# Performance work log

Measured on AMD Instinct MI355X. Metric: run time of the kernel, lower is better.

The kernel has to match this reference:

```python
import jax, jax.numpy as jnp
import numpy as np

INPUT_DIM = 1024
HIDDEN_DIM = 1024
BATCH = 8
SEQ = 2048


def setup_inputs() -> dict:
    key = jax.random.key(0)
    ks = jax.random.split(key, 7)
    s = 1.0 / np.sqrt(INPUT_DIM)
    return {
        "subgraph_embeddings": jax.random.normal(ks[0], (BATCH, SEQ, INPUT_DIM), dtype=jnp.float32),
        "Wq": jax.random.uniform(ks[1], (INPUT_DIM, HIDDEN_DIM), jnp.float32, -s, s),
        "bq": jax.random.uniform(ks[2], (HIDDEN_DIM,), jnp.float32, -s, s),
        "Wk": jax.random.uniform(ks[3], (INPUT_DIM, HIDDEN_DIM), jnp.float32, -s, s),
        "bk": jax.random.uniform(ks[4], (HIDDEN_DIM,), jnp.float32, -s, s),
        "Wv": jax.random.uniform(ks[5], (INPUT_DIM, HIDDEN_DIM), jnp.float32, -s, s),
        "bv": jax.random.uniform(ks[6], (HIDDEN_DIM,), jnp.float32, -s, s),
    }


def reference(subgraph_embeddings, Wq, bq, Wk, bk, Wv, bv):
    x = subgraph_embeddings  # [B, S, D]
    Q = jnp.einsum('bsd,dh->bsh', x, Wq) + bq
    K = jnp.einsum('bsd,dh->bsh', x, Wk) + bk
    V = jnp.einsum('bsd,dh->bsh', x, Wv) + bv
    scale = jnp.sqrt(jnp.float32(HIDDEN_DIM))
    scores = jnp.einsum('bqh,bkh->bqk', Q, K) / scale  # [B, S, S]
    weights = jax.nn.softmax(scores, axis=-1)
    return jnp.einsum('bqk,bkh->bqh', weights, V)
```

## Files before the change

### kernel.cpp

```cpp
#include <hip/hip_runtime.h>
#include <hip/hip_bf16.h>
#include <stdint.h>

typedef unsigned short u16;
typedef unsigned int u32;
typedef __attribute__((ext_vector_type(8))) short bf16x8;
typedef __attribute__((ext_vector_type(4))) float f32x4;

#define S_LEN 2048
#define D_DIM 1024
#define H_DIM 1024
#define BATCH 8
#define M_TOTAL (BATCH * S_LEN)

__device__ __forceinline__ u16 f2b(float f) {
  u32 u = __builtin_bit_cast(u32, f);
  u32 r = (u + 0x7fffu + ((u >> 16) & 1u)) >> 16;
  return (u16)r;
}

__global__ __launch_bounds__(256) void cast_x_kernel(const float* __restrict__ in,
                                                     u16* __restrict__ out, int n8) {
  int i = blockIdx.x * 256 + threadIdx.x;
  if (i >= n8) return;
  const float4* p = (const float4*)in;
  float4 a = p[2 * i], b = p[2 * i + 1];
  u32 w0 = (u32)f2b(a.x) | ((u32)f2b(a.y) << 16);
  u32 w1 = (u32)f2b(a.z) | ((u32)f2b(a.w) << 16);
  u32 w2 = (u32)f2b(b.x) | ((u32)f2b(b.y) << 16);
  u32 w3 = (u32)f2b(b.z) | ((u32)f2b(b.w) << 16);
  ((uint4*)out)[i] = make_uint4(w0, w1, w2, w3);
}

__global__ __launch_bounds__(256) void wcast_all_kernel(
    const float* __restrict__ Wq, const float* __restrict__ Wk,
    const float* __restrict__ Wv, const float* __restrict__ bq,
    const float* __restrict__ bk, u16* __restrict__ Wtqk,
    u16* __restrict__ Wtv, float* __restrict__ bqk, float* __restrict__ lsum) {
  __shared__ float tile[32][33];
  int z = blockIdx.z;
  const float* W = (z == 0) ? Wq : (z == 1) ? Wk : Wv;
  u16* Wt = (z == 0) ? Wtqk : (z == 1) ? (Wtqk + 1024 * 1024) : Wtv;
  int h0 = blockIdx.x * 32, d0 = blockIdx.y * 32;
  int tx = threadIdx.x & 31, ty = threadIdx.x >> 5;
#pragma unroll
  for (int r = ty; r < 32; r += 8)
    tile[r][tx] = W[(size_t)(d0 + r) * H_DIM + h0 + tx];
  if (blockIdx.x == 0 && blockIdx.y == 0) {
    if (z == 0) {
      for (int i = threadIdx.x; i < 1024; i += 256) bqk[i] = bq[i];
    } else if (z == 1) {
      for (int i = threadIdx.x; i < 1024; i += 256) bqk[1024 + i] = bk[i];
    } else {
      for (int i = threadIdx.x; i < M_TOTAL; i += 256) lsum[i] = 0.f;
    }
  }
  __syncthreads();
#pragma unroll
  for (int r = ty; r < 32; r += 8)
    Wt[(size_t)(h0 + r) * D_DIM + d0 + tx] = f2b(tile[tx][r]);
}

template <int BIAS, int EPI, bool OUT_BF16>
__global__ __launch_bounds__(512, 2) void gemm256(
    const u16* __restrict__ A, const u16* __restrict__ Bt, void* __restrict__ Cout,
    const float* __restrict__ bias, float* __restrict__ lsum,
    int M, int N, int K, int lda, int ldb, int ldc,
    long long aBatch, long long bBatch, long long cBatch, float scale) {
  __shared__ __align__(16) u16 As[2][256 * 64];
  __shared__ __align__(16) u16 Bs[2][256 * 64];
  const int tid = threadIdx.x;
  const int wave = tid >> 6, lane = tid & 63;
  const int quad = lane >> 4, lr = lane & 15;
  const int wm = (wave >> 2) * 128, wn = (wave & 3) * 64;
  const int row0 = blockIdx.x * 256, col0 = blockIdx.y * 256;
  A += (size_t)blockIdx.z * (size_t)aBatch;
  Bt += (size_t)blockIdx.z * (size_t)bBatch;

  f32x4 acc[8][4] = {};

  auto AsL = (__attribute__((address_space(3))) char*)&As[0][0];
  auto BsL = (__attribute__((address_space(3))) char*)&Bs[0][0];
  const char* Ab = (const char*)A;
  const char* Bb = (const char*)Bt;

  auto stage_aq = [&](int buf, int q, int k0) {
#pragma unroll
    for (int rr = 0; rr < 2; ++rr) {
      int idx = rr * 512 + tid;
      int i = idx >> 3, ch = idx & 7;
      int row = ((i >> 6) << 7) | (q << 6) | (i & 63);
      int cs = ch ^ (row & 7);
      const void* g = Ab + (((size_t)(row0 + row) * lda + (size_t)(k0 + cs * 8)) * 2);
      __builtin_amdgcn_global_load_lds(
          (const __attribute__((address_space(1))) void*)g,
          (__attribute__((address_space(3))) void*)(AsL + (size_t)buf * 32768 +
                                                   (size_t)(row * 8 + ch) * 16),
          16, 0, 0);
    }
  };
  auto stage_bq = [&](int buf, int q, int k0) {
#pragma unroll
    for (int rr = 0; rr < 2; ++rr) {
      int idx = rr * 512 + tid;
      int i = idx >> 3, ch = idx & 7;
      int row = ((i >> 5) << 6) | (q << 5) | (i & 31);
      int cs = ch ^ (row & 7);
      const void* g = Bb + (((size_t)(col0 + row) * ldb + (size_t)(k0 + cs * 8)) * 2);
      __builtin_amdgcn_global_load_lds(
          (const __attribute__((address_space(1))) void*)g,
          (__attribute__((address_space(3))) void*)(BsL + (size_t)buf * 32768 +
                                                   (size_t)(row * 8 + ch) * 16),
          16, 0, 0);
    }
  };

#define READ_A(MH)                                                              \
  _Pragma("unroll") for (int ksi = 0; ksi < 2; ++ksi)                           \
  _Pragma("unroll") for (int i = 0; i < 4; ++i) {                               \
    int r = wm + ((MH) * 4 + i) * 16 + lr;                                      \
    int cc = (ksi * 4 + quad) ^ (r & 7);                                        \
    afr[ksi][i] = *(const bf16x8*)&As[cur][r * 64 + cc * 8];                    \
  }
#define READ_B(NH)                                                              \
  _Pragma("unroll") for (int ksi = 0; ksi < 2; ++ksi)                           \
  _Pragma("unroll") for (int j = 0; j < 2; ++j) {                               \
    int r = wn + ((NH) * 2 + j) * 16 + lr;                                      \
    int cc = (ksi * 4 + quad) ^ (r & 7);                                        \
    bfr[NH][j][ksi] = *(const bf16x8*)&Bs[cur][r * 64 + cc * 8];                \
  }
#define MFMA_QUAD(MH, NH)                                                       \
  _Pragma("unroll") for (int ksi = 0; ksi < 2; ++ksi)                           \
  _Pragma("unroll") for (int i = 0; i < 4; ++i)                                 \
  _Pragma("unroll") for (int j = 0; j < 2; ++j)                                 \
    acc[(MH) * 4 + i][(NH) * 2 + j] = __builtin_amdgcn_mfma_f32_16x16x32_bf16(  \
        afr[ksi][i], bfr[NH][j][ksi], acc[(MH) * 4 + i][(NH) * 2 + j], 0, 0, 0);

#define BAR() __builtin_amdgcn_s_barrier()
#define WAIT_LGKM0()                                       \
  asm volatile("s_waitcnt lgkmcnt(0)" ::: "memory");       \
  __builtin_amdgcn_sched_barrier(0)
#define PRIO1() __builtin_amdgcn_s_setprio(1)
#define PRIO0() __builtin_amdgcn_s_setprio(0)

  const int nkt = K >> 6;

  stage_aq(0, 0, 0); stage_bq(0, 0, 0); stage_bq(0, 1, 0); stage_aq(0, 1, 0);
  stage_aq(1, 0, 64); stage_bq(1, 0, 64); stage_bq(1, 1, 64);
  asm volatile("s_waitcnt vmcnt(6)" ::: "memory");
  __builtin_amdgcn_sched_barrier(0);
  BAR();

  bf16x8 afr[2][4];
  bf16x8 bfr[2][2][2];

  for (int t = 0; t <= nkt - 3; ++t) {
    const int cur = t & 1, nxt = cur ^ 1;
    const int kn1 = (t + 1) << 6, kn2 = (t + 2) << 6;
    READ_A(0);
    READ_B(0);
    stage_aq(nxt, 1, kn1);
    asm volatile("s_waitcnt lgkmcnt(8)" ::: "memory");
    BAR();
    WAIT_LGKM0();
    PRIO1(); MFMA_QUAD(0, 0); PRIO0();
    BAR();
    READ_B(1);
    stage_aq(cur, 0, kn2);
    BAR();
    WAIT_LGKM0();
    PRIO1(); MFMA_QUAD(0, 1); PRIO0();
    BAR();
    READ_A(1);
    stage_bq(cur, 0, kn2);
    BAR();
    WAIT_LGKM0();
    PRIO1(); MFMA_QUAD(1, 0); PRIO0();
    BAR();
    stage_bq(cur, 1, kn2);
    BAR();
    PRIO1(); MFMA_QUAD(1, 1); PRIO0();
    asm volatile("s_waitcnt vmcnt(6)" ::: "memory");
    __builtin_amdgcn_sched_barrier(0);
    BAR();
  }
  {
    const int t = nkt - 2;
    const int cur = t & 1, nxt = cur ^ 1;
    const int kn1 = (t + 1) << 6;
    READ_A(0);
    READ_B(0);
    stage_aq(nxt, 1, kn1);
    asm volatile("s_waitcnt lgkmcnt(8)" ::: "memory");
    BAR();
    WAIT_LGKM0();
    PRIO1(); MFMA_QUAD(0, 0); PRIO0();
    BAR();
    READ_B(1);
    BAR();
    WAIT_LGKM0();
    PRIO1(); MFMA_QUAD(0, 1); PRIO0();
    BAR();
    READ_A(1);
    BAR();
    WAIT_LGKM0();
    PRIO1(); MFMA_QUAD(1, 0); PRIO0();
    BAR();
    PRIO1(); MFMA_QUAD(1, 1); PRIO0();
    asm volatile("s_waitcnt vmcnt(0)" ::: "memory");
    __builtin_amdgcn_sched_barrier(0);
    BAR();
  }
  {
    const int cur = (nkt - 1) & 1;
    READ_A(0);
    READ_B(0);
    MFMA_QUAD(0, 0);
    READ_B(1);
    MFMA_QUAD(0, 1);
    READ_A(1);
    MFMA_QUAD(1, 0);
    MFMA_QUAD(1, 1);
  }
#undef READ_A
#undef READ_B
#undef MFMA_QUAD
#undef BAR
#undef WAIT_LGKM0
#undef PRIO1
#undef PRIO0

  const long long lrow0 = (long long)blockIdx.z * M + row0;

  if constexpr (EPI == 1) {
    u16* C = (u16*)Cout + (size_t)blockIdx.z * (size_t)cBatch;
#pragma unroll
    for (int i = 0; i < 8; ++i) {
#pragma unroll
      for (int ii = 0; ii < 4; ++ii) {
        int r = wm + i * 16 + quad * 4 + ii;
        float rowsum = 0.f;
#pragma unroll
        for (int j = 0; j < 4; ++j) {
          float e = __expf(acc[i][j][ii] * scale);
          rowsum += e;
          C[(size_t)(row0 + r) * ldc + (col0 + wn + j * 16 + lr)] = f2b(e);
        }
#pragma unroll
        for (int off = 1; off < 16; off <<= 1) rowsum += __shfl_xor(rowsum, off);
        if (lr == 0) atomicAdd(lsum + lrow0 + r, rowsum);
      }
    }
    return;
  }

#pragma unroll
  for (int i = 0; i < 8; ++i) {
#pragma unroll
    for (int ii = 0; ii < 4; ++ii) {
      int r = wm + i * 16 + quad * 4 + ii;
      float radd = 0.f, rmul = 1.f;
      if (BIAS == 2) radd = bias[row0 + r];
      if (EPI == 2) rmul = 1.0f / lsum[lrow0 + r];
#pragma unroll
      for (int j = 0; j < 4; ++j) {
        int c = col0 + wn + j * 16 + lr;
        float v = acc[i][j][ii] * rmul + radd;
        if (BIAS == 1) v += bias[c];
        if constexpr (OUT_BF16) {
          u16* C = (u16*)Cout + (size_t)blockIdx.z * (size_t)cBatch;
          C[(size_t)(row0 + r) * ldc + c] = f2b(v);
        } else {
          float* C = (float*)Cout + (size_t)blockIdx.z * (size_t)cBatch;
          C[(size_t)(row0 + r) * ldc + c] = v;
        }
      }
    }
  }
}

extern "C" void kernel_launch(void* const* d_in, const int* in_sizes, int n_in,
                              void* d_out, int out_size, void* d_ws, size_t ws_size,
                              hipStream_t stream) {
  const float* x = (const float*)d_in[0];
  const float* Wq = (const float*)d_in[1];
  const float* bq = (const float*)d_in[2];
  const float* Wk = (const float*)d_in[3];
  const float* bk = (const float*)d_in[4];
  const float* Wv = (const float*)d_in[5];
  const float* bv = (const float*)d_in[6];
  float* out = (float*)d_out;

  char* ws = (char*)d_ws;
  u16* xb = (u16*)ws;   ws += (size_t)M_TOTAL * D_DIM * 2;
  u16* Wtqk = (u16*)ws; ws += (size_t)2 * H_DIM * D_DIM * 2;
  u16* Wtv = (u16*)ws;  ws += (size_t)H_DIM * D_DIM * 2;
  u16* QKm = (u16*)ws;  ws += (size_t)M_TOTAL * 2 * H_DIM * 2;
  u16* Vt = (u16*)ws;   ws += (size_t)BATCH * H_DIM * S_LEN * 2;
  u16* Sm = (u16*)ws;   ws += (size_t)BATCH * S_LEN * S_LEN * 2;
  float* bqk = (float*)ws;  ws += 2048 * 4;
  float* lsum = (float*)ws; ws += (size_t)M_TOTAL * 4;

  cast_x_kernel<<<(M_TOTAL * D_DIM / 8 + 255) / 256, 256, 0, stream>>>(
      x, xb, M_TOTAL * D_DIM / 8);
  wcast_all_kernel<<<dim3(32, 32, 3), 256, 0, stream>>>(
      Wq, Wk, Wv, bq, bk, Wtqk, Wtv, bqk, lsum);

  gemm256<1, 0, true><<<dim3(64, 8, 1), 512, 0, stream>>>(
      xb, Wtqk, QKm, bqk, nullptr, M_TOTAL, 2 * H_DIM, D_DIM,
      D_DIM, D_DIM, 2 * H_DIM, 0, 0, 0, 0.f);

  gemm256<2, 0, true><<<dim3(4, 8, BATCH), 512, 0, stream>>>(
      Wtv, xb, Vt, bv, nullptr, H_DIM, S_LEN, D_DIM,
      D_DIM, D_DIM, S_LEN,
      0LL, (long long)S_LEN * D_DIM, (long long)H_DIM * S_LEN, 0.f);

  gemm256<0, 1, true><<<dim3(8, 8, BATCH), 512, 0, stream>>>(
      QKm, QKm + H_DIM, Sm, nullptr, lsum, S_LEN, S_LEN, H_DIM,
      2 * H_DIM, 2 * H_DIM, S_LEN,
      (long long)S_LEN * 2 * H_DIM, (long long)S_LEN * 2 * H_DIM,
      (long long)S_LEN * S_LEN, 0.03125f);

  gemm256<0, 2, false><<<dim3(8, 4, BATCH), 512, 0, stream>>>(
      Sm, Vt, out, nullptr, lsum, S_LEN, H_DIM, S_LEN,
      S_LEN, S_LEN, H_DIM,
      (long long)S_LEN * S_LEN, (long long)H_DIM * S_LEN,
      (long long)S_LEN * H_DIM, 0.f);
}
```

Before: 396.3 us.

## Double-buffer GEMM register fragments to overlap LDS reads with MFMA

Restructures the GEMM main loop so A/B fragments are held in two register sets (a0/a1, b0/b1). The next tile's first fragments are prefetched from LDS during the current tile's MFMAs, and waits use partial lgkmcnt counts instead of full drains. Global-to-LDS staging is reordered so the whole next A tile is staged in the prologue and the vmcnt wait moves mid-iteration. This aims to hide LDS read latency behind matrix math. The cost is higher register pressure and tighter reliance on correct counter values.

```diff
diff --git a/kernel.cpp b/kernel.cpp
--- a/kernel.cpp
+++ b/kernel.cpp
@@ -115,30 +115,30 @@
     }
   };
 
-#define READ_A(MH)                                                              \
+#define READ_A(dst, MH, BUF)                                                    \
   _Pragma("unroll") for (int ksi = 0; ksi < 2; ++ksi)                           \
   _Pragma("unroll") for (int i = 0; i < 4; ++i) {                               \
     int r = wm + ((MH) * 4 + i) * 16 + lr;                                      \
     int cc = (ksi * 4 + quad) ^ (r & 7);                                        \
-    afr[ksi][i] = *(const bf16x8*)&As[cur][r * 64 + cc * 8];                    \
-  }
-#define READ_B(NH)                                                              \
+    dst[ksi][i] = *(const bf16x8*)&As[BUF][r * 64 + cc * 8];                    \
+  }
+#define READ_B(dst, NH, BUF)                                                    \
   _Pragma("unroll") for (int ksi = 0; ksi < 2; ++ksi)                           \
   _Pragma("unroll") for (int j = 0; j < 2; ++j) {                               \
     int r = wn + ((NH) * 2 + j) * 16 + lr;                                      \
     int cc = (ksi * 4 + quad) ^ (r & 7);                                        \
-    bfr[NH][j][ksi] = *(const bf16x8*)&Bs[cur][r * 64 + cc * 8];                \
-  }
-#define MFMA_QUAD(MH, NH)                                                       \
+    dst[ksi][j] = *(const bf16x8*)&Bs[BUF][r * 64 + cc * 8];                    \
+  }
+#define MFMA_Q(Af, Bf, MH, NH)                                                  \
   _Pragma("unroll") for (int ksi = 0; ksi < 2; ++ksi)                           \
   _Pragma("unroll") for (int i = 0; i < 4; ++i)                                 \
   _Pragma("unroll") for (int j = 0; j < 2; ++j)                                 \
     acc[(MH) * 4 + i][(NH) * 2 + j] = __builtin_amdgcn_mfma_f32_16x16x32_bf16(  \
-        afr[ksi][i], bfr[NH][j][ksi], acc[(MH) * 4 + i][(NH) * 2 + j], 0, 0, 0);
+        Af[ksi][i], Bf[ksi][j], acc[(MH) * 4 + i][(NH) * 2 + j], 0, 0, 0);
 
 #define BAR() __builtin_amdgcn_s_barrier()
-#define WAIT_LGKM0()                                       \
-  asm volatile("s_waitcnt lgkmcnt(0)" ::: "memory");       \
+#define LGKM(N)                                                  \
+  asm volatile("s_waitcnt lgkmcnt(" #N ")" ::: "memory");        \
   __builtin_amdgcn_sched_barrier(0)
 #define PRIO1() __builtin_amdgcn_s_setprio(1)
 #define PRIO0() __builtin_amdgcn_s_setprio(0)
@@ -146,87 +146,87 @@
   const int nkt = K >> 6;
 
   stage_aq(0, 0, 0); stage_bq(0, 0, 0); stage_bq(0, 1, 0); stage_aq(0, 1, 0);
-  stage_aq(1, 0, 64); stage_bq(1, 0, 64); stage_bq(1, 1, 64);
-  asm volatile("s_waitcnt vmcnt(6)" ::: "memory");
+  stage_aq(1, 0, 64); stage_bq(1, 0, 64); stage_bq(1, 1, 64); stage_aq(1, 1, 64);
+  asm volatile("s_waitcnt vmcnt(8)" ::: "memory");
   __builtin_amdgcn_sched_barrier(0);
   BAR();
 
-  bf16x8 afr[2][4];
-  bf16x8 bfr[2][2][2];
+  bf16x8 a0[2][4], a1[2][4];
+  bf16x8 b0[2][2], b1[2][2];
+
+  READ_A(a0, 0, 0);
+  READ_B(b0, 0, 0);
 
   for (int t = 0; t <= nkt - 3; ++t) {
     const int cur = t & 1, nxt = cur ^ 1;
-    const int kn1 = (t + 1) << 6, kn2 = (t + 2) << 6;
-    READ_A(0);
-    READ_B(0);
-    stage_aq(nxt, 1, kn1);
-    asm volatile("s_waitcnt lgkmcnt(8)" ::: "memory");
-    BAR();
-    WAIT_LGKM0();
-    PRIO1(); MFMA_QUAD(0, 0); PRIO0();
-    BAR();
-    READ_B(1);
+    const int kn2 = (t + 2) << 6;
+    READ_B(b1, 1, cur);
+    BAR();
+    LGKM(4);
+    PRIO1(); MFMA_Q(a0, b0, 0, 0); PRIO0();
+    BAR();
+    READ_A(a1, 1, cur);
     stage_aq(cur, 0, kn2);
     BAR();
-    WAIT_LGKM0();
-    PRIO1(); MFMA_QUAD(0, 1); PRIO0();
-    BAR();
-    READ_A(1);
+    LGKM(8);
+    PRIO1(); MFMA_Q(a0, b1, 0, 1); PRIO0();
+    asm volatile("s_waitcnt vmcnt(2)" ::: "memory");
+    __builtin_amdgcn_sched_barrier(0);
+    BAR();
+    READ_A(a0, 0, nxt);
     stage_bq(cur, 0, kn2);
     BAR();
-    WAIT_LGKM0();
-    PRIO1(); MFMA_QUAD(1, 0); PRIO0();
-    BAR();
+    LGKM(8);
+    PRIO1(); MFMA_Q(a1, b0, 1, 0); PRIO0();
+    BAR();
+    READ_B(b0, 0, nxt);
     stage_bq(cur, 1, kn2);
-    BAR();
-    PRIO1(); MFMA_QUAD(1, 1); PRIO0();
-    asm volatile("s_waitcnt vmcnt(6)" ::: "memory");
-    __builtin_amdgcn_sched_barrier(0);
+    stage_aq(cur, 1, kn2);
+    BAR();
+    PRIO1(); MFMA_Q(a1, b1, 1, 1); PRIO0();
     BAR();
   }
   {
-    const int t = nkt - 2;
-    const int cur = t & 1, nxt = cur ^ 1;
-    const int kn1 = (t + 1) << 6;
-    READ_A(0);
-    READ_B(0);
-    stage_aq(nxt, 1, kn1);
-    asm volatile("s_waitcnt lgkmcnt(8)" ::: "memory");
-    BAR();
-    WAIT_LGKM0();
-    PRIO1(); MFMA_QUAD(0, 0); PRIO0();
-    BAR();
-    READ_B(1);
-    BAR();
-    WAIT_LGKM0();
-    PRIO1(); MFMA_QUAD(0, 1); PRIO0();
-    BAR();
-    READ_A(1);
-    BAR();
-    WAIT_LGKM0();
-    PRIO1(); MFMA_QUAD(1, 0); PRIO0();
-    BAR();
-    PRIO1(); MFMA_QUAD(1, 1); PRIO0();
+    const int cur = (nkt - 2) & 1, nxt = cur ^ 1;
+    READ_B(b1, 1, cur);
+    BAR();
+    LGKM(4);
+    PRIO1(); MFMA_Q(a0, b0, 0, 0); PRIO0();
+    BAR();
+    READ_A(a1, 1, cur);
+    BAR();
+    LGKM(8);
+    PRIO1(); MFMA_Q(a0, b1, 0, 1); PRIO0();
     asm volatile("s_waitcnt vmcnt(0)" ::: "memory");
     __builtin_amdgcn_sched_barrier(0);
     BAR();
+    READ_A(a0, 0, nxt);
+    BAR();
+    LGKM(8);
+    PRIO1(); MFMA_Q(a1, b0, 1, 0); PRIO0();
+    BAR();
+    READ_B(b0, 0, nxt);
+    BAR();
+    PRIO1(); MFMA_Q(a1, b1, 1, 1); PRIO0();
+    BAR();
   }
   {
     const int cur = (nkt - 1) & 1;
-    READ_A(0);
-    READ_B(0);
-    MFMA_QUAD(0, 0);
-    READ_B(1);
-    MFMA_QUAD(0, 1);
-    READ_A(1);
-    MFMA_QUAD(1, 0);
-    MFMA_QUAD(1, 1);
+    READ_B(b1, 1, cur);
+    LGKM(4);
+    MFMA_Q(a0, b0, 0, 0);
+    READ_A(a1, 1, cur);
+    LGKM(8);
+    MFMA_Q(a0, b1, 0, 1);
+    LGKM(0);
+    MFMA_Q(a1, b0, 1, 0);
+    MFMA_Q(a1, b1, 1, 1);
   }
 #undef READ_A
 #undef READ_B
-#undef MFMA_QUAD
+#undef MFMA_Q
 #undef BAR
-#undef WAIT_LGKM0
+#undef LGKM
 #undef PRIO1
 #undef PRIO0
 
```

New measurement: 439.2 us. 1.11x slower.
